# Optimization experiments

Hardware: AMD Instinct MI355X
Metric: run time of the kernel (lower is better)

## Reference

```python
import jax, jax.numpy as jnp
import numpy as np

N, D, H, E, TOP_K = 8192, 1024, 4096, 8, 2


def setup_inputs() -> dict:
    key = jax.random.key(0)
    ks = jax.random.split(key, 6)
    input_batch = jax.random.normal(ks[0], (N, D), dtype=jnp.float32)
    # Router-style top-k: distinct expert ids per token, softmax-normalized weights
    logits = jax.random.normal(ks[1], (N, E), dtype=jnp.float32)
    topk_vals, indices = jax.lax.top_k(logits, TOP_K)          # [N, k]
    probabilities = jax.nn.softmax(topk_vals, axis=-1)          # [N, k]
    scale1 = 1.0 / np.sqrt(D)
    scale2 = 1.0 / np.sqrt(H)
    W1 = jax.random.normal(ks[2], (E, D, H), dtype=jnp.float32) * scale1
    b1 = jnp.zeros((E, H), dtype=jnp.float32)
    W2 = jax.random.normal(ks[3], (E, H, D), dtype=jnp.float32) * scale2
    b2 = jnp.zeros((E, D), dtype=jnp.float32)
    return {
        "input_batch": input_batch,
        "probabilities": probabilities,
        "indices": indices.astype(jnp.int64),
        "W1": W1, "b1": b1, "W2": W2, "b2": b2,
    }


def reference(input_batch, probabilities, indices, W1, b1, W2, b2):
    # Each expert is Linear(D->H) + ReLU + Linear(H->D).
    # Dense per-expert forward (batched GEMM over the expert axis), then
    # gather the top_k selected expert outputs per token and combine with
    # router probabilities applied AFTER the experts:
    #   out[n] = sum_k p[n,k] * expert_{idx[n,k]}(x[n])
    h = jax.nn.relu(jnp.einsum("nd,edh->enh", input_batch, W1) + b1[:, None, :])
    y = jnp.einsum("enh,eho->eno", h, W2) + b2[:, None, :]      # [E, N, D]
    y_tok = jnp.swapaxes(y, 0, 1)                                # [N, E, D]
    sel = jnp.take_along_axis(y_tok, indices[:, :, None], axis=1)  # [N, k, D]
    output = jnp.sum(probabilities[:, :, None] * sel, axis=1)    # [N, D]
    total_loss = jnp.asarray(0.0, dtype=input_batch.dtype)       # sampler+expert losses are zero here
    return output, total_loss
```

## Files before the change

### kernel.cpp

```cpp
#include <hip/hip_runtime.h>
#include <hip/hip_bf16.h>

#define N_TOK 8192
#define DDIM 1024
#define HDIM 4096
#define NEXP 8
#define TOPK 2
#define NK (N_TOK*TOPK)
#define BM 128
#define BK 32
#define MAXT 136

typedef __hip_bfloat16 bf16;
typedef __attribute__((ext_vector_type(8))) short bf16x8;
typedef __attribute__((ext_vector_type(4))) float f32x4;

__device__ __forceinline__ void gload16(const void* g, void* lds) {
  auto l = (__attribute__((address_space(3))) unsigned int*)(unsigned int)(unsigned long long)lds;
  auto gg = (const __attribute__((address_space(1))) unsigned int*)(unsigned long long)g;
  __builtin_amdgcn_global_load_lds(gg, l, 16, 0, 0);
}

__global__ void k_count(const int* __restrict__ idx, int stride,
                        int* __restrict__ cnt) {
  int r = blockIdx.x * blockDim.x + threadIdx.x;
  if (r >= NK) return;
  int e = idx[r * stride];
  e = min(max(e, 0), NEXP - 1);
  atomicAdd(&cnt[e], 1);
}

__global__ void k_scan(const int* __restrict__ cnt, int* __restrict__ offp,
                       int* __restrict__ off2, int* __restrict__ texp,
                       int* __restrict__ tok) {
  __shared__ int so[NEXP + 1], sc[NEXP];
  int tid = threadIdx.x;
  if (tid == 0) {
    int cum = 0;
    for (int e = 0; e < NEXP; e++) {
      so[e] = cum; sc[e] = cnt[e];
      cum += ((cnt[e] + BM - 1) / BM) * BM;
    }
    so[NEXP] = cum;
    for (int e = 0; e <= NEXP; e++) offp[e] = so[e];
  }
  __syncthreads();
  if (tid < NEXP) off2[tid] = so[tid];
  int total_tiles = so[NEXP] / BM;
  for (int t = tid; t < MAXT; t += blockDim.x) {
    int e = -1;
    if (t < total_tiles) {
      for (int q = 0; q < NEXP; q++)
        if (t * BM >= so[q] && t * BM < so[q + 1]) e = q;
    }
    texp[t] = e;
  }
  for (int e = 0; e < NEXP; e++) {
    int start = so[e] + sc[e], end = so[e + 1];
    for (int i = start + tid; i < end; i += blockDim.x) tok[i] = 0;
  }
}

__global__ void k_scatter(const int* __restrict__ idx, int stride,
                          int* __restrict__ off2, int* __restrict__ tok,
                          int* __restrict__ pos) {
  int r = blockIdx.x * blockDim.x + threadIdx.x;
  if (r >= NK) return;
  int e = idx[r * stride];
  e = min(max(e, 0), NEXP - 1);
  int p = atomicAdd(&off2[e], 1);
  tok[p] = r >> 1;
  pos[r] = p;
}

__global__ void k_cvt_x(const float* __restrict__ x, bf16* __restrict__ xb) {
  int i = blockIdx.x * blockDim.x + threadIdx.x;
  if (i >= N_TOK * DDIM / 8) return;
  float4 a = ((const float4*)x)[(size_t)i * 2];
  float4 b = ((const float4*)x)[(size_t)i * 2 + 1];
  union { bf16 h[8]; uint4 v; } u;
  u.h[0] = __float2bfloat16(a.x); u.h[1] = __float2bfloat16(a.y);
  u.h[2] = __float2bfloat16(a.z); u.h[3] = __float2bfloat16(a.w);
  u.h[4] = __float2bfloat16(b.x); u.h[5] = __float2bfloat16(b.y);
  u.h[6] = __float2bfloat16(b.z); u.h[7] = __float2bfloat16(b.w);
  *(uint4*)&xb[(size_t)i * 8] = u.v;
}

__global__ void k_transpose(const float* __restrict__ in, bf16* __restrict__ out,
                            int R, int C) {
  __shared__ float t[32][65];
  size_t ebase = (size_t)blockIdx.z * R * C;
  int r0 = blockIdx.y * 32, c0 = blockIdx.x * 64;
  int tid = threadIdx.x;
  {
    int lr = tid >> 3, lc = (tid & 7) * 8;
    const float4* src = (const float4*)&in[ebase + (size_t)(r0 + lr) * C + c0 + lc];
    float4 a = src[0], b = src[1];
    t[lr][lc + 0] = a.x; t[lr][lc + 1] = a.y; t[lr][lc + 2] = a.z; t[lr][lc + 3] = a.w;
    t[lr][lc + 4] = b.x; t[lr][lc + 5] = b.y; t[lr][lc + 6] = b.z; t[lr][lc + 7] = b.w;
  }
  __syncthreads();
  {
    int sc = tid >> 2, sr = (tid & 3) * 8;
    union { bf16 h[8]; uint4 v; } u;
#pragma unroll
    for (int j = 0; j < 8; j++) u.h[j] = __float2bfloat16(t[sr + j][sc]);
    *(uint4*)&out[ebase + (size_t)(c0 + sc) * R + r0 + sr] = u.v;
  }
}

template<int MODE>
__global__ __launch_bounds__(512, 4) void k_gemm(
    const bf16* __restrict__ A, const bf16* __restrict__ Bt,
    const float* __restrict__ bias, const int* __restrict__ texp,
    const int* __restrict__ tok, int tile_base, void* __restrict__ Cout)
{
  constexpr int KT   = MODE ? HDIM : DDIM;
  constexpr int NCOL = MODE ? DDIM : HDIM;
  constexpr int BN   = 256;
  constexpr int GX   = NCOL / BN;
  constexpr int NT   = KT / BK;
  constexpr int BUFB = (BM + BN) * BK * 2;

  int nwg = gridDim.x, orig = blockIdx.x;
  int q8 = nwg >> 3, r8 = nwg & 7;
  int xcd = orig & 7, jj0 = orig >> 3;
  int w = (xcd < r8 ? xcd * (q8 + 1) : r8 * (q8 + 1) + (xcd - r8) * q8) + jj0;
  int tn = w % GX;
  int tmr = w / GX;
  int tm = tile_base + tmr;
  int e = texp[tm];
  if (e < 0) return;

  int tid = threadIdx.x, lane = tid & 63, wid = tid >> 6;
  int wm = wid >> 2, wn = wid & 3;
  int lr = lane & 15, kg = lane >> 4;

  __shared__ __align__(16) char lds[3 * BUFB];

  unsigned goff[3];
  {
    int row = tid >> 2, c = tid & 3;
    int ch = c ^ ((row >> 1) & 3);
    int arow = MODE ? (tmr * BM + row) : tok[tm * BM + row];
    goff[0] = (unsigned)(arow * KT + ch * 8);
    goff[1] = (unsigned)((e * NCOL + tn * BN + row) * KT + ch * 8);
    goff[2] = (unsigned)((e * NCOL + tn * BN + 128 + row) * KT + ch * 8);
  }

  auto stage = [&](int kt, int buf) {
    char* base = lds + buf * BUFB;
    gload16(A + goff[0] + kt * BK, base + tid * 16);
    gload16(Bt + goff[1] + kt * BK, base + 8192 + tid * 16);
    gload16(Bt + goff[2] + kt * BK, base + 16384 + tid * 16);
  };

  f32x4 acc[4][4];
#pragma unroll
  for (int i = 0; i < 4; i++)
#pragma unroll
    for (int j = 0; j < 4; j++) acc[i][j] = (f32x4){0.f, 0.f, 0.f, 0.f};

  stage(0, 0);
  stage(1, 1);
  asm volatile("s_waitcnt vmcnt(3)" ::: "memory");
  __builtin_amdgcn_s_barrier();

#pragma unroll 1
  for (int kt = 0; kt < NT; ++kt) {
    if (kt + 2 < NT) stage(kt + 2, (kt + 2) % 3);

    const char* base = lds + (kt % 3) * BUFB;
    bf16x8 av[4], bv[4];
#pragma unroll
    for (int mi = 0; mi < 4; ++mi) {
      int m = wm * 64 + mi * 16 + lr;
      int slot = kg ^ ((m >> 1) & 3);
      av[mi] = *(const bf16x8*)(base + m * 64 + slot * 16);
    }
#pragma unroll
    for (int ni = 0; ni < 4; ++ni) {
      int n = wn * 64 + ni * 16 + lr;
      int slot = kg ^ ((n >> 1) & 3);
      bv[ni] = *(const bf16x8*)(base + 8192 + n * 64 + slot * 16);
    }

#pragma unroll
    for (int mi = 0; mi < 4; ++mi)
#pragma unroll
      for (int ni = 0; ni < 4; ++ni)
        acc[mi][ni] = __builtin_amdgcn_mfma_f32_16x16x32_bf16(
            av[mi], bv[ni], acc[mi][ni], 0, 0, 0);

    if (kt + 1 < NT) {
      if (kt + 2 < NT) asm volatile("s_waitcnt vmcnt(3)" ::: "memory");
      else             asm volatile("s_waitcnt vmcnt(0)" ::: "memory");
      __builtin_amdgcn_s_barrier();
    }
  }

  const float* be = bias + (size_t)e * NCOL;
  int crow0 = (MODE ? tm : tmr) * BM;
#pragma unroll
  for (int ni = 0; ni < 4; ++ni) {
    int n = tn * BN + wn * 64 + ni * 16 + lr;
    float bvv = be[n];
#pragma unroll
    for (int mi = 0; mi < 4; ++mi) {
#pragma unroll
      for (int j = 0; j < 4; j++) {
        int mrow = wm * 64 + mi * 16 + kg * 4 + j;
        float v = acc[mi][ni][j] + bvv;
        if (MODE == 0) v = fmaxf(v, 0.f);
        ((bf16*)Cout)[(size_t)(crow0 + mrow) * NCOL + n] = __float2bfloat16(v);
      }
    }
  }
}

__global__ void k_combine(const bf16* __restrict__ y, const float* __restrict__ prob,
                          const int* __restrict__ pos, float* __restrict__ out) {
  int gid = blockIdx.x * blockDim.x + threadIdx.x;
  if (gid >= N_TOK * DDIM / 8) return;
  int n = gid >> 7;
  int d8 = gid & 127;
  int r0 = pos[2 * n], r1 = pos[2 * n + 1];
  float p0 = prob[2 * n], p1 = prob[2 * n + 1];
  uint4 a = *(const uint4*)&y[(size_t)r0 * DDIM + d8 * 8];
  uint4 b = *(const uint4*)&y[(size_t)r1 * DDIM + d8 * 8];
  const unsigned short* ah = (const unsigned short*)&a;
  const unsigned short* bh = (const unsigned short*)&b;
  float o[8];
#pragma unroll
  for (int k = 0; k < 8; k++) {
    float fa = __uint_as_float((unsigned)ah[k] << 16);
    float fb = __uint_as_float((unsigned)bh[k] << 16);
    o[k] = p0 * fa + p1 * fb;
  }
  float4* op = (float4*)&out[(size_t)n * DDIM + d8 * 8];
  op[0] = (float4){o[0], o[1], o[2], o[3]};
  op[1] = (float4){o[4], o[5], o[6], o[7]};
  if (gid == 0) out[(size_t)N_TOK * DDIM] = 0.f;
}

extern "C" void kernel_launch(void* const* d_in, const int* in_sizes, int n_in,
                              void* d_out, int out_size, void* d_ws, size_t ws_size,
                              hipStream_t stream) {
  const float* x    = (const float*)d_in[0];
  const float* prob = (const float*)d_in[1];
  const int*   idx  = (const int*)d_in[2];
  const float* W1   = (const float*)d_in[3];
  const float* b1   = (const float*)d_in[4];
  const float* W2   = (const float*)d_in[5];
  const float* b2   = (const float*)d_in[6];
  float* out = (float*)d_out;
  int stride = (in_sizes[2] == NK) ? 1 : 2;

  char* ws = (char*)d_ws;
  size_t cur = 0;
  auto alloc = [&](size_t bytes) -> void* {
    cur = (cur + 255) & ~(size_t)255;
    void* p = ws + cur; cur += bytes; return p;
  };
  int* cnt   = (int*)alloc(NEXP * 4);
  int* offp  = (int*)alloc((NEXP + 1) * 4);
  int* off2  = (int*)alloc(NEXP * 4);
  int* texp  = (int*)alloc(MAXT * 4);
  int* tok   = (int*)alloc((size_t)MAXT * BM * 4);
  int* pos   = (int*)alloc((size_t)NK * 4);
  bf16* Xb   = (bf16*)alloc((size_t)N_TOK * DDIM * 2);
  bf16* W1t  = (bf16*)alloc((size_t)NEXP * HDIM * DDIM * 2);
  bf16* W2t  = (bf16*)alloc((size_t)NEXP * DDIM * HDIM * 2);
  bf16* ybuf = (bf16*)alloc((size_t)MAXT * BM * DDIM * 2);
  cur = (cur + 255) & ~(size_t)255;
  size_t h_off = cur;
  size_t h_avail = ws_size > h_off ? ws_size - h_off : 0;
  long long ts_ll = (long long)(h_avail / ((size_t)BM * HDIM * 2));
  int ts = (int)(ts_ll < 1 ? 1 : (ts_ll > MAXT ? MAXT : ts_ll));
  bf16* hbuf = (bf16*)(ws + h_off);

  hipMemsetAsync(cnt, 0, NEXP * 4, stream);
  k_count<<<(NK + 255) / 256, 256, 0, stream>>>(idx, stride, cnt);
  k_scan<<<1, 256, 0, stream>>>(cnt, offp, off2, texp, tok);
  k_scatter<<<(NK + 255) / 256, 256, 0, stream>>>(idx, stride, off2, tok, pos);
  k_cvt_x<<<(N_TOK * DDIM / 8 + 255) / 256, 256, 0, stream>>>(x, Xb);
  k_transpose<<<dim3(HDIM / 64, DDIM / 32, NEXP), 256, 0, stream>>>(W1, W1t, DDIM, HDIM);
  k_transpose<<<dim3(DDIM / 64, HDIM / 32, NEXP), 256, 0, stream>>>(W2, W2t, HDIM, DDIM);

  for (int base = 0; base < MAXT; base += ts) {
    int cnt_t = (MAXT - base < ts) ? (MAXT - base) : ts;
    k_gemm<0><<<dim3(cnt_t * (HDIM / 256)), 512, 0, stream>>>(
        Xb, W1t, b1, texp, tok, base, (void*)hbuf);
    k_gemm<1><<<dim3(cnt_t * (DDIM / 256)), 512, 0, stream>>>(
        hbuf, W2t, b2, texp, tok, base, (void*)ybuf);
  }
  k_combine<<<(N_TOK * DDIM / 8 + 255) / 256, 256, 0, stream>>>(ybuf, prob, pos, out);
}
```

Measured before the change: 582.5 us.

## Load B operand directly from global into registers, keep only A in LDS

```diff
diff --git a/kernel.cpp b/kernel.cpp
--- a/kernel.cpp
+++ b/kernel.cpp
@@ -110,7 +110,7 @@
 }
 
 template<int MODE>
-__global__ __launch_bounds__(512, 4) void k_gemm(
+__global__ __launch_bounds__(512, 2) void k_gemm(
     const bf16* __restrict__ A, const bf16* __restrict__ Bt,
     const float* __restrict__ bias, const int* __restrict__ texp,
     const int* __restrict__ tok, int tile_base, void* __restrict__ Cout)
@@ -120,7 +120,7 @@
   constexpr int BN   = 256;
   constexpr int GX   = NCOL / BN;
   constexpr int NT   = KT / BK;
-  constexpr int BUFB = (BM + BN) * BK * 2;
+  constexpr int ABUF = BM * BK * 2;
 
   int nwg = gridDim.x, orig = blockIdx.x;
   int q8 = nwg >> 3, r8 = nwg & 7;
@@ -136,66 +136,92 @@
   int wm = wid >> 2, wn = wid & 3;
   int lr = lane & 15, kg = lane >> 4;
 
-  __shared__ __align__(16) char lds[3 * BUFB];
-
-  unsigned goff[3];
+  __shared__ __align__(16) char lds[3 * ABUF];
+
+  unsigned aoff;
   {
     int row = tid >> 2, c = tid & 3;
     int ch = c ^ ((row >> 1) & 3);
     int arow = MODE ? (tmr * BM + row) : tok[tm * BM + row];
-    goff[0] = (unsigned)(arow * KT + ch * 8);
-    goff[1] = (unsigned)((e * NCOL + tn * BN + row) * KT + ch * 8);
-    goff[2] = (unsigned)((e * NCOL + tn * BN + 128 + row) * KT + ch * 8);
-  }
-
-  auto stage = [&](int kt, int buf) {
-    char* base = lds + buf * BUFB;
-    gload16(A + goff[0] + kt * BK, base + tid * 16);
-    gload16(Bt + goff[1] + kt * BK, base + 8192 + tid * 16);
-    gload16(Bt + goff[2] + kt * BK, base + 16384 + tid * 16);
+    aoff = (unsigned)(arow * KT + ch * 8);
+  }
+  auto stageA = [&](int kt, int buf) {
+    gload16(A + aoff + kt * BK, lds + buf * ABUF + tid * 16);
   };
 
+  const bf16* bp0 = Bt + (size_t)(e * NCOL + tn * BN + wn * 64 + lr) * KT + kg * 8;
+  const bf16* bp1 = bp0 + (size_t)16 * KT;
+  const bf16* bp2 = bp0 + (size_t)32 * KT;
+  const bf16* bp3 = bp0 + (size_t)48 * KT;
+
   f32x4 acc[4][4];
 #pragma unroll
   for (int i = 0; i < 4; i++)
 #pragma unroll
     for (int j = 0; j < 4; j++) acc[i][j] = (f32x4){0.f, 0.f, 0.f, 0.f};
 
-  stage(0, 0);
-  stage(1, 1);
-  asm volatile("s_waitcnt vmcnt(3)" ::: "memory");
-  __builtin_amdgcn_s_barrier();
-
-#pragma unroll 1
-  for (int kt = 0; kt < NT; ++kt) {
-    if (kt + 2 < NT) stage(kt + 2, (kt + 2) % 3);
-
-    const char* base = lds + (kt % 3) * BUFB;
-    bf16x8 av[4], bv[4];
+  auto readA = [&](int buf, bf16x8* av) {
+    const char* base = lds + buf * ABUF;
 #pragma unroll
     for (int mi = 0; mi < 4; ++mi) {
       int m = wm * 64 + mi * 16 + lr;
       int slot = kg ^ ((m >> 1) & 3);
       av[mi] = *(const bf16x8*)(base + m * 64 + slot * 16);
     }
-#pragma unroll
-    for (int ni = 0; ni < 4; ++ni) {
-      int n = wn * 64 + ni * 16 + lr;
-      int slot = kg ^ ((n >> 1) & 3);
-      bv[ni] = *(const bf16x8*)(base + 8192 + n * 64 + slot * 16);
-    }
-
+  };
+  auto mfma16 = [&](bf16x8* av, bf16x8* bv) {
 #pragma unroll
     for (int mi = 0; mi < 4; ++mi)
 #pragma unroll
       for (int ni = 0; ni < 4; ++ni)
         acc[mi][ni] = __builtin_amdgcn_mfma_f32_16x16x32_bf16(
             av[mi], bv[ni], acc[mi][ni], 0, 0, 0);
-
-    if (kt + 1 < NT) {
-      if (kt + 2 < NT) asm volatile("s_waitcnt vmcnt(3)" ::: "memory");
-      else             asm volatile("s_waitcnt vmcnt(0)" ::: "memory");
+  };
+
+  bf16x8 bva[4], bvb[4], av[4];
+
+  stageA(0, 0);
+  stageA(1, 1);
+  asm volatile("s_waitcnt vmcnt(0)" ::: "memory");
+  bva[0] = *(const bf16x8*)(bp0);
+  bva[1] = *(const bf16x8*)(bp1);
+  bva[2] = *(const bf16x8*)(bp2);
+  bva[3] = *(const bf16x8*)(bp3);
+  __builtin_amdgcn_s_barrier();
+  __builtin_amdgcn_sched_barrier(0);
+
+#pragma unroll 1
+  for (int it = 0; it < NT / 2; ++it) {
+    int kt = 2 * it;
+
+    if (kt + 2 < NT) stageA(kt + 2, (kt + 2) % 3);
+    {
+      int o = (kt + 1) * BK;
+      bvb[0] = *(const bf16x8*)(bp0 + o);
+      bvb[1] = *(const bf16x8*)(bp1 + o);
+      bvb[2] = *(const bf16x8*)(bp2 + o);
+      bvb[3] = *(const bf16x8*)(bp3 + o);
+    }
+    readA(kt % 3, av);
+    mfma16(av, bva);
+    asm volatile("s_waitcnt vmcnt(5)" ::: "memory");
+    __builtin_amdgcn_s_barrier();
+    __builtin_amdgcn_sched_barrier(0);
+
+    if (kt + 3 < NT) stageA(kt + 3, (kt + 3) % 3);
+    if (kt + 2 < NT) {
+      int o = (kt + 2) * BK;
+      bva[0] = *(const bf16x8*)(bp0 + o);
+      bva[1] = *(const bf16x8*)(bp1 + o);
+      bva[2] = *(const bf16x8*)(bp2 + o);
+      bva[3] = *(const bf16x8*)(bp3 + o);
+    }
+    readA((kt + 1) % 3, av);
+    mfma16(av, bvb);
+    if (kt + 2 < NT) {
+      asm volatile("s_waitcnt vmcnt(5)" ::: "memory");
       __builtin_amdgcn_s_barrier();
+      __builtin_amdgcn_sched_barrier(0);
     }
   }
 
```

Result: slower. 971.9 us (+66.8%).
